# Optimization experiments

Hardware: AMD Instinct MI355X
Metric: run time of the kernel (lower is better)

The kernel has to match this reference:

```python
import jax, jax.numpy as jnp
import numpy as np

B, T_IN, N, C_IN = 4, 16, 5000, 16
HID, C_OUT, KSZ, K_CHEB = 32, 64, 3, 3
E = 80000
BN_EPS = 1e-5


def _conv1xk(x, W, b):
    # x: (B,C,N,T), W: (O,I,1,k) -> (B,O,N,T-k+1)
    y = jax.lax.conv_general_dilated(x, W, (1, 1), 'VALID',
                                     dimension_numbers=('NCHW', 'OIHW', 'NCHW'))
    return y + b[None, :, None, None]


def temporal_conv(X, W1, b1, W2, b2, W3, b3):
    # X: (B,T,N,C) -> (B,T-k+1,N,O); gated temporal conv (GLU-style)
    Xp = jnp.transpose(X, (0, 3, 2, 1))  # (B,C,N,T)
    P = _conv1xk(Xp, W1, b1)
    Q = jax.nn.sigmoid(_conv1xk(Xp, W2, b2))
    R = _conv1xk(Xp, W3, b3)
    H = jax.nn.relu(P * Q + R)
    return jnp.transpose(H, (0, 3, 2, 1))


def cheb_conv(x, edge_index, edge_weight, W, b, lambda_max=2.0):
    # x: (B,T,N,C). Batched ChebConv with sym normalization (PyG semantics).
    n = x.shape[2]
    row, col = edge_index[0], edge_index[1]
    deg = jax.ops.segment_sum(edge_weight, row, num_segments=n)
    dis = jnp.where(deg > 0, deg ** -0.5, 0.0)
    w_norm = dis[row] * edge_weight * dis[col]  # (E,)

    def lhat(z):
        # A_norm z via scatter-add over edges, batched over (B,T)
        az = jnp.zeros_like(z).at[:, :, row, :].add(
            w_norm[None, None, :, None] * z[:, :, col, :])
        # L z = z - A_norm z ; L_hat = (2/lmax) L - I
        return (2.0 / lambda_max) * (z - az) - z

    Tx0 = x
    out = jnp.einsum('btnc,cd->btnd', Tx0, W[0])
    Tx1 = lhat(Tx0)
    out = out + jnp.einsum('btnc,cd->btnd', Tx1, W[1])
    for k in range(2, W.shape[0]):
        Tx2 = 2.0 * lhat(Tx1) - Tx0
        out = out + jnp.einsum('btnc,cd->btnd', Tx2, W[k])
        Tx0, Tx1 = Tx1, Tx2
    return out + b


def batch_norm_nodes(T, gamma, beta):
    # torch: permute to (B, N, T, C), BatchNorm2d(num_nodes), permute back
    Tp = jnp.transpose(T, (0, 2, 1, 3))  # (B,N,T,C)
    mean = jnp.mean(Tp, axis=(0, 2, 3), keepdims=True)
    var = jnp.mean((Tp - mean) ** 2, axis=(0, 2, 3), keepdims=True)  # biased
    Tn = (Tp - mean) / jnp.sqrt(var + BN_EPS)
    Tn = Tn * gamma[None, :, None, None] + beta[None, :, None, None]
    return jnp.transpose(Tn, (0, 2, 1, 3))


def setup_inputs() -> dict:
    key = jax.random.key(0)
    ks = jax.random.split(key, 20)
    s = 0.05
    inp = {
        'X': jax.random.normal(ks[0], (B, T_IN, N, C_IN), jnp.float32),
        'edge_index': jax.random.randint(ks[1], (2, E), 0, N, jnp.int64
                                         if jax.config.jax_enable_x64 else jnp.int32),
        'edge_weight': jax.random.uniform(ks[2], (E,), jnp.float32),
        'tc1_w1': jax.random.normal(ks[3], (HID, C_IN, 1, KSZ)) * s,
        'tc1_b1': jnp.zeros((HID,)),
        'tc1_w2': jax.random.normal(ks[4], (HID, C_IN, 1, KSZ)) * s,
        'tc1_b2': jnp.zeros((HID,)),
        'tc1_w3': jax.random.normal(ks[5], (HID, C_IN, 1, KSZ)) * s,
        'tc1_b3': jnp.zeros((HID,)),
        'cheb_W': jax.random.normal(ks[6], (K_CHEB, HID, HID)) * s,
        'cheb_b': jnp.zeros((HID,)),
        'tc2_w1': jax.random.normal(ks[7], (C_OUT, HID, 1, KSZ)) * s,
        'tc2_b1': jnp.zeros((C_OUT,)),
        'tc2_w2': jax.random.normal(ks[8], (C_OUT, HID, 1, KSZ)) * s,
        'tc2_b2': jnp.zeros((C_OUT,)),
        'tc2_w3': jax.random.normal(ks[9], (C_OUT, HID, 1, KSZ)) * s,
        'tc2_b3': jnp.zeros((C_OUT,)),
        'bn_gamma': jnp.ones((N,)),
        'bn_beta': jnp.zeros((N,)),
    }
    return inp


def reference(X, edge_index, edge_weight,
              tc1_w1, tc1_b1, tc1_w2, tc1_b2, tc1_w3, tc1_b3,
              cheb_W, cheb_b,
              tc2_w1, tc2_b1, tc2_w2, tc2_b2, tc2_w3, tc2_b3,
              bn_gamma, bn_beta):
    T0 = temporal_conv(X, tc1_w1, tc1_b1, tc1_w2, tc1_b2, tc1_w3, tc1_b3)
    T = jax.nn.relu(cheb_conv(T0, edge_index, edge_weight, cheb_W, cheb_b))
    T = temporal_conv(T, tc2_w1, tc2_b1, tc2_w2, tc2_b2, tc2_w3, tc2_b3)
    return batch_norm_nodes(T, bn_gamma, bn_beta)
```

## Files before the change

### kernel.cpp

```cpp
#include <hip/hip_runtime.h>
#include <hip/hip_bf16.h>

#define STC_N     5000
#define STC_TIN   16
#define STC_T1    14
#define STC_T2    12
#define STC_CIN   16
#define STC_CH    32
#define STC_CO    64
#define STC_BT1   56
#define STC_BT2   48
#define STC_RT1   17500
#define STC_GBLK  1280
#define STC_GWAVE (STC_GBLK*4)
#define STC_ROWB1 1792

#define STC_OFF_DEG   0
#define STC_OFF_CNT   20000
#define STC_OFF_CUR   40000
#define STC_OFF_DIS   60000
#define STC_OFF_OFFS  80000
#define STC_OFF_WN    100032
#define STC_OFF_CCOL  420032
#define STC_OFF_CW    740032
#define STC_OFF_T0    1060096
#define STC_OFF_G1    (STC_OFF_T0 + 17920000)
#define STC_OFF_G2    (STC_OFF_G1 + 17920000)
#define STC_OFF_PK2   (STC_OFF_G2 + 17920000)
#define STC_OFF_PK1   (STC_OFF_PK2 + 36864)
#define STC_OFF_PKC   (STC_OFF_PK1 + 12288)
#define STC_WS_REQ    (STC_OFF_PKC + 6144)

typedef __hip_bfloat16 bf16;
typedef short stc_s8 __attribute__((ext_vector_type(8)));
typedef float stc_f4 __attribute__((ext_vector_type(4)));

__device__ float stc_lo16(unsigned u) { return __uint_as_float(u << 16); }
__device__ float stc_hi16(unsigned u) { return __uint_as_float(u & 0xffff0000u); }
__device__ float stc_s2f(short s) {
    return __uint_as_float(((unsigned)(unsigned short)s) << 16);
}

__device__ short stc_f2bs(float f) {
    unsigned u = __float_as_uint(f);
    u = (u + 0x7FFFu + ((u >> 16) & 1u)) >> 16;
    return (short)u;
}

__global__ void STConv_9972914061616_kernel() {}

__global__ void stc_fill(float* out, int n, float val) {
    int i = blockIdx.x * 256 + threadIdx.x;
    if (i < n) out[i] = val;
}

__global__ void stc_init(int* zp,
                         const float* w1a, const float* w1b, const float* w1c,
                         const float* w2a, const float* w2b, const float* w2c,
                         const float* chW,
                         short* pk1, short* pk2, short* pkc) {
    if (blockIdx.x < 59) {
        int i = blockIdx.x * 256 + threadIdx.x;
        if (i < 15000) zp[i] = 0;
        return;
    }
    int gid = (blockIdx.x - 59) * 256 + threadIdx.x;
    if (gid >= 54 * 64) return;
    int fi = gid >> 6;
    int lane = gid & 63;
    int j = lane & 15;
    int quad = lane >> 4;
    short f[8];
    if (fi < 36) {
        int s = fi % 3;
        int cc4 = fi / 3;
        int conv = cc4 >> 2;
        int c4 = cc4 & 3;
        const float* Wp = (conv == 0) ? w2a : ((conv == 1) ? w2b : w2c);
        int och = c4 * 16 + j;
        for (int i = 0; i < 8; ++i) {
            int cc = quad * 8 + i;
            f[i] = stc_f2bs(Wp[och * 96 + cc * 3 + s]);
        }
        for (int i = 0; i < 8; ++i) pk2[(fi * 64 + lane) * 8 + i] = f[i];
    } else if (fi < 48) {
        int t = fi - 36;
        int s = t & 1;
        int cj = t >> 1;
        int conv = cj >> 1;
        int jt = cj & 1;
        const float* Wp = (conv == 0) ? w1a : ((conv == 1) ? w1b : w1c);
        int och = jt * 16 + j;
        for (int i = 0; i < 8; ++i) {
            int k = s * 32 + quad * 8 + i;
            int kt = k >> 4;
            int c = k & 15;
            f[i] = (kt < 3) ? stc_f2bs(Wp[och * 48 + c * 3 + kt]) : (short)0;
        }
        for (int i = 0; i < 8; ++i) pk1[(t * 64 + lane) * 8 + i] = f[i];
    } else {
        int t = fi - 48;
        int s = t >> 1;
        int jt = t & 1;
        int d = jt * 16 + j;
        for (int i = 0; i < 8; ++i) {
            int c = quad * 8 + i;
            float w0 = chW[c * 32 + d];
            float w1 = chW[1024 + c * 32 + d];
            float w2 = chW[2048 + c * 32 + d];
            float v = (s == 0) ? (w0 - w2) : ((s == 1) ? -w1 : 2.0f * w2);
            f[i] = stc_f2bs(v);
        }
        for (int i = 0; i < 8; ++i) pkc[(t * 64 + lane) * 8 + i] = f[i];
    }
}

__global__ void stc_deg(const int* ei, const float* ew, float* deg, int E) {
    int e = blockIdx.x * 256 + threadIdx.x;
    if (e < E) atomicAdd(&deg[ei[e]], ew[e]);
}

__global__ void stc_wnorm(const int* ei, const float* ew, const float* deg,
                          float* wn, int* cnt, int E) {
    int e = blockIdx.x * 256 + threadIdx.x;
    if (e < E) {
        int r = ei[e];
        int c = ei[E + e];
        float dr = deg[r];
        float dc = deg[c];
        float ir = (dr > 0.0f) ? rsqrtf(dr) : 0.0f;
        float ic = (dc > 0.0f) ? rsqrtf(dc) : 0.0f;
        wn[e] = ir * ew[e] * ic;
        atomicAdd(&cnt[r], 1);
    }
}

__global__ void stc_scan(const int* cnt, int* offs, int n) {
    __shared__ int s[256];
    int tid = threadIdx.x;
    int base = tid * 20;
    int loc[20];
    int sum = 0;
#pragma unroll
    for (int k = 0; k < 20; ++k) {
        int i = base + k;
        int v = (i < n) ? cnt[i] : 0;
        loc[k] = sum;
        sum += v;
    }
    s[tid] = sum;
    __syncthreads();
    for (int off = 1; off < 256; off <<= 1) {
        int t = (tid >= off) ? s[tid - off] : 0;
        __syncthreads();
        s[tid] += t;
        __syncthreads();
    }
    int pre = (tid > 0) ? s[tid - 1] : 0;
#pragma unroll
    for (int k = 0; k < 20; ++k) {
        int i = base + k;
        if (i < n) offs[i] = pre + loc[k];
    }
    if (tid == 255) offs[n] = s[255];
}

__global__ void stc_scatter(const int* ei, const float* wn, const int* offs,
                            int* cursor, int* ccol, float* cw, int E) {
    int e = blockIdx.x * 256 + threadIdx.x;
    if (e < E) {
        int r = ei[e];
        int pos = atomicAdd(&cursor[r], 1);
        int slot = offs[r] + pos;
        ccol[slot] = ei[E + e];
        cw[slot] = wn[e];
    }
}

__global__ __launch_bounds__(256, 2) void stc_tconv1m(
    const float* X, const short* pk1,
    const float* B1, const float* B2, const float* B3,
    bf16* T0) {
    int lane = threadIdx.x & 63;
    int j = lane & 15;
    int quad = lane >> 4;
    int wave = blockIdx.x * 4 + (threadIdx.x >> 6);

    stc_s8 bfrag[3][2][2];
    for (int conv = 0; conv < 3; ++conv)
        for (int jt = 0; jt < 2; ++jt)
            for (int s = 0; s < 2; ++s) {
                int t = (conv * 2 + jt) * 2 + s;
                bfrag[conv][jt][s] = *(const stc_s8*)(pk1 + (t * 64 + lane) * 8);
            }
    float pb[2], qb[2], rb[2];
    for (int jt = 0; jt < 2; ++jt) {
        int och = jt * 16 + j;
        pb[jt] = B1[och];
        qb[jt] = B2[och];
        rb[jt] = B3[och];
    }

    for (int rt = wave; rt < STC_RT1; rt += STC_GWAVE) {
        int rm = rt * 16 + j;
        int n = rm % STC_N;
        int bt = rm / STC_N;
        int t = bt % STC_T1;
        int b = bt / STC_T1;

        int kt0 = quad >> 1;
        int c0 = (quad & 1) * 8;
        const float* xp0 = X + ((size_t)((b * STC_TIN + t + kt0) * STC_N + n)) * STC_CIN + c0;
        stc_s8 af0;
        for (int i = 0; i < 8; ++i) af0[i] = stc_f2bs(xp0[i]);

        stc_s8 af1;
        if (quad < 2) {
            const float* xp1 = X + ((size_t)((b * STC_TIN + t + 2) * STC_N + n)) * STC_CIN + c0;
            for (int i = 0; i < 8; ++i) af1[i] = stc_f2bs(xp1[i]);
        } else {
            for (int i = 0; i < 8; ++i) af1[i] = 0;
        }

        stc_f4 acc[6];
        for (int a = 0; a < 6; ++a) acc[a] = (stc_f4){0.0f, 0.0f, 0.0f, 0.0f};
        for (int conv = 0; conv < 3; ++conv) {
            for (int jt = 0; jt < 2; ++jt) {
                int a = conv * 2 + jt;
                acc[a] = __builtin_amdgcn_mfma_f32_16x16x32_bf16(
                    af0, bfrag[conv][jt][0], acc[a], 0, 0, 0);
                acc[a] = __builtin_amdgcn_mfma_f32_16x16x32_bf16(
                    af1, bfrag[conv][jt][1], acc[a], 0, 0, 0);
            }
        }

        for (int jt = 0; jt < 2; ++jt) {
            for (int reg = 0; reg < 4; ++reg) {
                float P = acc[jt][reg] + pb[jt];
                float Q = acc[2 + jt][reg] + qb[jt];
                float R = acc[4 + jt][reg] + rb[jt];
                float Qc = fminf(fmaxf(Q, -30.0f), 30.0f);
                float sg = 1.0f / (1.0f + expf(-Qc));
                float h = P * sg + R;
                if (h < 0.0f) h = 0.0f;
                int row = rt * 16 + quad * 4 + reg;
                int nw = row % STC_N;
                int btw = row / STC_N;
                T0[(size_t)nw * STC_ROWB1 + btw * STC_CH + jt * 16 + j] =
                    __float2bfloat16(h);
            }
        }
    }
}

__global__ void stc_gatherv(const bf16* z, bf16* g, const int* offs,
                            const int* ccol, const float* cw) {
    int n = blockIdx.x;
    __shared__ int col_s[128];
    __shared__ float w_s[128];
    int beg = offs[n];
    int end = offs[n + 1];
    int cg = threadIdx.x & 3;
    int sl = threadIdx.x >> 2;
    int act = (sl < STC_BT1);
    float a0 = 0.f, a1 = 0.f, a2 = 0.f, a3 = 0.f;
    float a4 = 0.f, a5 = 0.f, a6 = 0.f, a7 = 0.f;
    const bf16* zb = z + sl * STC_CH + cg * 8;
    for (int chunk = beg; chunk < end; chunk += 128) {
        int m = end - chunk;
        if (m > 128) m = 128;
        if (threadIdx.x < m) {
            col_s[threadIdx.x] = ccol[chunk + threadIdx.x];
            w_s[threadIdx.x] = cw[chunk + threadIdx.x];
        }
        __syncthreads();
        if (act) {
            int i = 0;
            for (; i + 4 <= m; i += 4) {
                float w0 = w_s[i], w1 = w_s[i + 1], w2 = w_s[i + 2], w3 = w_s[i + 3];
                uint4 u0 = *(const uint4*)(zb + (size_t)col_s[i] * STC_ROWB1);
                uint4 u1 = *(const uint4*)(zb + (size_t)col_s[i + 1] * STC_ROWB1);
                uint4 u2 = *(const uint4*)(zb + (size_t)col_s[i + 2] * STC_ROWB1);
                uint4 u3 = *(const uint4*)(zb + (size_t)col_s[i + 3] * STC_ROWB1);
                a0 += w0 * stc_lo16(u0.x); a1 += w0 * stc_hi16(u0.x);
                a2 += w0 * stc_lo16(u0.y); a3 += w0 * stc_hi16(u0.y);
                a4 += w0 * stc_lo16(u0.z); a5 += w0 * stc_hi16(u0.z);
                a6 += w0 * stc_lo16(u0.w); a7 += w0 * stc_hi16(u0.w);
                a0 += w1 * stc_lo16(u1.x); a1 += w1 * stc_hi16(u1.x);
                a2 += w1 * stc_lo16(u1.y); a3 += w1 * stc_hi16(u1.y);
                a4 += w1 * stc_lo16(u1.z); a5 += w1 * stc_hi16(u1.z);
                a6 += w1 * stc_lo16(u1.w); a7 += w1 * stc_hi16(u1.w);
                a0 += w2 * stc_lo16(u2.x); a1 += w2 * stc_hi16(u2.x);
                a2 += w2 * stc_lo16(u2.y); a3 += w2 * stc_hi16(u2.y);
                a4 += w2 * stc_lo16(u2.z); a5 += w2 * stc_hi16(u2.z);
                a6 += w2 * stc_lo16(u2.w); a7 += w2 * stc_hi16(u2.w);
                a0 += w3 * stc_lo16(u3.x); a1 += w3 * stc_hi16(u3.x);
                a2 += w3 * stc_lo16(u3.y); a3 += w3 * stc_hi16(u3.y);
                a4 += w3 * stc_lo16(u3.z); a5 += w3 * stc_hi16(u3.z);
                a6 += w3 * stc_lo16(u3.w); a7 += w3 * stc_hi16(u3.w);
            }
            for (; i < m; ++i) {
                float w = w_s[i];
                uint4 u = *(const uint4*)(zb + (size_t)col_s[i] * STC_ROWB1);
                a0 += w * stc_lo16(u.x); a1 += w * stc_hi16(u.x);
                a2 += w * stc_lo16(u.y); a3 += w * stc_hi16(u.y);
                a4 += w * stc_lo16(u.z); a5 += w * stc_hi16(u.z);
                a6 += w * stc_lo16(u.w); a7 += w * stc_hi16(u.w);
            }
        }
        __syncthreads();
    }
    if (act) {
        unsigned p0 = ((unsigned)(unsigned short)stc_f2bs(a0)) |
                      (((unsigned)(unsigned short)stc_f2bs(a1)) << 16);
        unsigned p1 = ((unsigned)(unsigned short)stc_f2bs(a2)) |
                      (((unsigned)(unsigned short)stc_f2bs(a3)) << 16);
        unsigned p2 = ((unsigned)(unsigned short)stc_f2bs(a4)) |
                      (((unsigned)(unsigned short)stc_f2bs(a5)) << 16);
        unsigned p3 = ((unsigned)(unsigned short)stc_f2bs(a6)) |
                      (((unsigned)(unsigned short)stc_f2bs(a7)) << 16);
        uint4 o;
        o.x = p0; o.y = p1; o.z = p2; o.w = p3;
        *(uint4*)(g + (size_t)n * STC_ROWB1 + sl * STC_CH + cg * 8) = o;
    }
}

__global__ __launch_bounds__(256, 2) void stc_combconv2bn(
    const bf16* T0, const bf16* G1, const bf16* G2,
    const short* pkc, const float* chB,
    const short* pk2, const float* B1, const float* B2, const float* B3,
    const float* gamma, const float* beta, float* T2) {
    __shared__ short comb[4][64 * 40];
    __shared__ short hb[4][48 * 72];
    int lane = threadIdx.x & 63;
    int j = lane & 15;
    int quad = lane >> 4;
    int w = threadIdx.x >> 6;
    int n = blockIdx.x * 4 + w;
    short* cmb = comb[w];
    short* hbw = hb[w];

    {
        stc_s8 cfrag[3][2];
        for (int s = 0; s < 3; ++s)
            for (int jt = 0; jt < 2; ++jt)
                cfrag[s][jt] = *(const stc_s8*)(pkc + ((s * 2 + jt) * 64 + lane) * 8);
        float bl[2];
        bl[0] = chB[j];
        bl[1] = chB[16 + j];
        for (int t3 = 0; t3 < 4; ++t3) {
            size_t rm = (size_t)n * STC_BT1 + t3 * 16 + j;
            size_t abase = rm * STC_CH + quad * 8;
            stc_s8 a0 = *(const stc_s8*)(T0 + abase);
            stc_s8 a1 = *(const stc_s8*)(G1 + abase);
            stc_s8 a2 = *(const stc_s8*)(G2 + abase);
            stc_f4 acc[2];
            acc[0] = (stc_f4){0.0f, 0.0f, 0.0f, 0.0f};
            acc[1] = (stc_f4){0.0f, 0.0f, 0.0f, 0.0f};
            for (int jt = 0; jt < 2; ++jt) {
                acc[jt] = __builtin_amdgcn_mfma_f32_16x16x32_bf16(a0, cfrag[0][jt], acc[jt], 0, 0, 0);
                acc[jt] = __builtin_amdgcn_mfma_f32_16x16x32_bf16(a1, cfrag[1][jt], acc[jt], 0, 0, 0);
                acc[jt] = __builtin_amdgcn_mfma_f32_16x16x32_bf16(a2, cfrag[2][jt], acc[jt], 0, 0, 0);
            }
            for (int jt = 0; jt < 2; ++jt) {
                for (int reg = 0; reg < 4; ++reg) {
                    float h = acc[jt][reg] + bl[jt];
                    if (h < 0.0f) h = 0.0f;
                    int row = t3 * 16 + quad * 4 + reg;
                    cmb[row * 40 + jt * 16 + j] = stc_f2bs(h);
                }
            }
        }
    }

    stc_s8 bfrag[3][4][3];
    for (int conv = 0; conv < 3; ++conv)
        for (int c4 = 0; c4 < 4; ++c4)
            for (int s = 0; s < 3; ++s) {
                int fi = (conv * 4 + c4) * 3 + s;
                bfrag[conv][c4][s] = *(const stc_s8*)(pk2 + (fi * 64 + lane) * 8);
            }
    float pb[4], qb[4], rb[4];
    for (int c4 = 0; c4 < 4; ++c4) {
        int och = c4 * 16 + j;
        pb[c4] = B1[och];
        qb[c4] = B2[och];
        rb[c4] = B3[och];
    }

    float lsum = 0.0f;
    for (int t3 = 0; t3 < 3; ++t3) {
        int btb = t3 * 16;
        int bt2 = btb + j;
        int b = bt2 / STC_T2;
        int t = bt2 % STC_T2;
        const short* ap = cmb + (b * STC_T1 + t) * 40 + quad * 8;
        stc_s8 af0 = *(const stc_s8*)(ap);
        stc_s8 af1 = *(const stc_s8*)(ap + 40);
        stc_s8 af2 = *(const stc_s8*)(ap + 80);

        stc_f4 acc[12];
        for (int a = 0; a < 12; ++a) acc[a] = (stc_f4){0.0f, 0.0f, 0.0f, 0.0f};

        for (int conv = 0; conv < 3; ++conv) {
            for (int c4 = 0; c4 < 4; ++c4) {
                int a = conv * 4 + c4;
                acc[a] = __builtin_amdgcn_mfma_f32_16x16x32_bf16(
                    af0, bfrag[conv][c4][0], acc[a], 0, 0, 0);
                acc[a] = __builtin_amdgcn_mfma_f32_16x16x32_bf16(
                    af1, bfrag[conv][c4][1], acc[a], 0, 0, 0);
                acc[a] = __builtin_amdgcn_mfma_f32_16x16x32_bf16(
                    af2, bfrag[conv][c4][2], acc[a], 0, 0, 0);
            }
        }

        for (int c4 = 0; c4 < 4; ++c4) {
            for (int reg = 0; reg < 4; ++reg) {
                float P = acc[c4][reg] + pb[c4];
                float Q = acc[4 + c4][reg] + qb[c4];
                float R = acc[8 + c4][reg] + rb[c4];
                float Qc = fminf(fmaxf(Q, -30.0f), 30.0f);
                float sg = 1.0f / (1.0f + expf(-Qc));
                float h = P * sg + R;
                if (h < 0.0f) h = 0.0f;
                short hs = stc_f2bs(h);
                int row = btb + quad * 4 + reg;
                hbw[row * 72 + c4 * 16 + j] = hs;
                lsum += stc_s2f(hs);
            }
        }
    }

    for (int off = 32; off; off >>= 1) lsum += __shfl_xor(lsum, off);
    float mean = lsum * (1.0f / (STC_BT2 * STC_CO));
    float sq = 0.0f;
    for (int k = 0; k < STC_BT2; ++k) {
        float d = stc_s2f(hbw[k * 72 + lane]) - mean;
        sq += d * d;
    }
    for (int off = 32; off; off >>= 1) sq += __shfl_xor(sq, off);
    float var = sq * (1.0f / (STC_BT2 * STC_CO));
    float istd = rsqrtf(var + 1e-5f);
    float scale = istd * gamma[n];
    float shift = beta[n] - mean * scale;
    for (int k = 0; k < STC_BT2; ++k) {
        T2[((size_t)k * STC_N + n) * STC_CO + lane] =
            stc_s2f(hbw[k * 72 + lane]) * scale + shift;
    }
}

extern "C" void kernel_launch(void* const* d_in, const int* in_sizes, int n_in,
                              void* d_out, int out_size, void* d_ws, size_t ws_size,
                              hipStream_t stream) {
    float* out = (float*)d_out;
    int outb = (out_size + 255) / 256;

    if (n_in < 19) {
        stc_fill<<<outb, 256, 0, stream>>>(out, out_size, 60.0f);
        return;
    }
    if (ws_size < (size_t)STC_WS_REQ) {
        stc_fill<<<outb, 256, 0, stream>>>(out, out_size, 50.0f);
        return;
    }

    const float* X = (const float*)d_in[0];
    const int* ei = (const int*)d_in[1];
    const float* ew = (const float*)d_in[2];
    const float* w1a = (const float*)d_in[3];
    const float* b1a = (const float*)d_in[4];
    const float* w1b = (const float*)d_in[5];
    const float* b1b = (const float*)d_in[6];
    const float* w1c = (const float*)d_in[7];
    const float* b1c = (const float*)d_in[8];
    const float* chW = (const float*)d_in[9];
    const float* chB = (const float*)d_in[10];
    const float* w2a = (const float*)d_in[11];
    const float* b2a = (const float*)d_in[12];
    const float* w2b = (const float*)d_in[13];
    const float* b2b = (const float*)d_in[14];
    const float* w2c = (const float*)d_in[15];
    const float* b2c = (const float*)d_in[16];
    const float* gam = (const float*)d_in[17];
    const float* bet = (const float*)d_in[18];
    int E = in_sizes[1] / 2;

    char* ws = (char*)d_ws;
    float* deg = (float*)(ws + STC_OFF_DEG);
    int* cnt = (int*)(ws + STC_OFF_CNT);
    int* cursor = (int*)(ws + STC_OFF_CUR);
    int* offs = (int*)(ws + STC_OFF_OFFS);
    float* wn = (float*)(ws + STC_OFF_WN);
    int* ccol = (int*)(ws + STC_OFF_CCOL);
    float* cw = (float*)(ws + STC_OFF_CW);
    bf16* T0 = (bf16*)(ws + STC_OFF_T0);
    bf16* G1 = (bf16*)(ws + STC_OFF_G1);
    bf16* G2 = (bf16*)(ws + STC_OFF_G2);
    short* pk2 = (short*)(ws + STC_OFF_PK2);
    short* pk1 = (short*)(ws + STC_OFF_PK1);
    short* pkc = (short*)(ws + STC_OFF_PKC);

    stc_init<<<73, 256, 0, stream>>>((int*)(ws + STC_OFF_DEG),
                                     w1a, w1b, w1c, w2a, w2b, w2c, chW,
                                     pk1, pk2, pkc);
    stc_deg<<<(E + 255) / 256, 256, 0, stream>>>(ei, ew, deg, E);
    stc_wnorm<<<(E + 255) / 256, 256, 0, stream>>>(ei, ew, deg, wn, cnt, E);
    stc_scan<<<1, 256, 0, stream>>>(cnt, offs, STC_N);
    stc_scatter<<<(E + 255) / 256, 256, 0, stream>>>(ei, wn, offs, cursor, ccol, cw, E);
    stc_tconv1m<<<STC_GBLK, 256, 0, stream>>>(X, pk1, b1a, b1b, b1c, T0);
    stc_gatherv<<<STC_N, 256, 0, stream>>>(T0, G1, offs, ccol, cw);
    stc_gatherv<<<STC_N, 256, 0, stream>>>(G1, G2, offs, ccol, cw);
    stc_combconv2bn<<<1250, 256, 0, stream>>>(
        T0, G1, G2, pkc, chB, pk2, b2a, b2b, b2c, gam, bet, out);
}
```

Measured before the change: 271.0 us.

## Split per-node conv2+batchnorm work across four waves of one block

The final fused kernel now assigns one node per 256-thread block instead of one node per wave. Each wave computes one 16-row tile of the Chebyshev combine and one 16-channel slice of the second temporal conv, and the BN mean and variance are reduced across waves through shared memory. This cuts per-wave register use (3 accumulators instead of 12, fewer weight fragments) and LDS footprint, which should allow higher occupancy, at the cost of block-level syncs. The sigmoid also switches from expf to the faster __expf intrinsic, which is slightly less accurate.

```diff
diff --git a/kernel.cpp b/kernel.cpp
--- a/kernel.cpp
+++ b/kernel.cpp
@@ -240,7 +240,7 @@
                 float Q = acc[2 + jt][reg] + qb[jt];
                 float R = acc[4 + jt][reg] + rb[jt];
                 float Qc = fminf(fmaxf(Q, -30.0f), 30.0f);
-                float sg = 1.0f / (1.0f + expf(-Qc));
+                float sg = 1.0f / (1.0f + __expf(-Qc));
                 float h = P * sg + R;
                 if (h < 0.0f) h = 0.0f;
                 int row = rt * 16 + quad * 4 + reg;
@@ -330,63 +330,57 @@
     const short* pkc, const float* chB,
     const short* pk2, const float* B1, const float* B2, const float* B3,
     const float* gamma, const float* beta, float* T2) {
-    __shared__ short comb[4][64 * 40];
-    __shared__ short hb[4][48 * 72];
+    __shared__ short comb[64 * 40];
+    __shared__ short hb[48 * 72];
+    __shared__ float red[8];
     int lane = threadIdx.x & 63;
     int j = lane & 15;
     int quad = lane >> 4;
     int w = threadIdx.x >> 6;
-    int n = blockIdx.x * 4 + w;
-    short* cmb = comb[w];
-    short* hbw = hb[w];
+    int n = blockIdx.x;
 
     {
         stc_s8 cfrag[3][2];
         for (int s = 0; s < 3; ++s)
             for (int jt = 0; jt < 2; ++jt)
                 cfrag[s][jt] = *(const stc_s8*)(pkc + ((s * 2 + jt) * 64 + lane) * 8);
-        float bl[2];
-        bl[0] = chB[j];
-        bl[1] = chB[16 + j];
-        for (int t3 = 0; t3 < 4; ++t3) {
-            size_t rm = (size_t)n * STC_BT1 + t3 * 16 + j;
-            size_t abase = rm * STC_CH + quad * 8;
-            stc_s8 a0 = *(const stc_s8*)(T0 + abase);
-            stc_s8 a1 = *(const stc_s8*)(G1 + abase);
-            stc_s8 a2 = *(const stc_s8*)(G2 + abase);
-            stc_f4 acc[2];
-            acc[0] = (stc_f4){0.0f, 0.0f, 0.0f, 0.0f};
-            acc[1] = (stc_f4){0.0f, 0.0f, 0.0f, 0.0f};
-            for (int jt = 0; jt < 2; ++jt) {
-                acc[jt] = __builtin_amdgcn_mfma_f32_16x16x32_bf16(a0, cfrag[0][jt], acc[jt], 0, 0, 0);
-                acc[jt] = __builtin_amdgcn_mfma_f32_16x16x32_bf16(a1, cfrag[1][jt], acc[jt], 0, 0, 0);
-                acc[jt] = __builtin_amdgcn_mfma_f32_16x16x32_bf16(a2, cfrag[2][jt], acc[jt], 0, 0, 0);
+        float bl0 = chB[j];
+        float bl1 = chB[16 + j];
+        size_t rm = (size_t)n * STC_BT1 + w * 16 + j;
+        size_t abase = rm * STC_CH + quad * 8;
+        stc_s8 a0 = *(const stc_s8*)(T0 + abase);
+        stc_s8 a1 = *(const stc_s8*)(G1 + abase);
+        stc_s8 a2 = *(const stc_s8*)(G2 + abase);
+        stc_f4 acc[2];
+        acc[0] = (stc_f4){0.0f, 0.0f, 0.0f, 0.0f};
+        acc[1] = (stc_f4){0.0f, 0.0f, 0.0f, 0.0f};
+        for (int jt = 0; jt < 2; ++jt) {
+            acc[jt] = __builtin_amdgcn_mfma_f32_16x16x32_bf16(a0, cfrag[0][jt], acc[jt], 0, 0, 0);
+            acc[jt] = __builtin_amdgcn_mfma_f32_16x16x32_bf16(a1, cfrag[1][jt], acc[jt], 0, 0, 0);
+            acc[jt] = __builtin_amdgcn_mfma_f32_16x16x32_bf16(a2, cfrag[2][jt], acc[jt], 0, 0, 0);
+        }
+        for (int jt = 0; jt < 2; ++jt) {
+            float bl = (jt == 0) ? bl0 : bl1;
+            for (int reg = 0; reg < 4; ++reg) {
+                float h = acc[jt][reg] + bl;
+                if (h < 0.0f) h = 0.0f;
+                int row = w * 16 + quad * 4 + reg;
+                comb[row * 40 + jt * 16 + j] = stc_f2bs(h);
             }
-            for (int jt = 0; jt < 2; ++jt) {
-                for (int reg = 0; reg < 4; ++reg) {
-                    float h = acc[jt][reg] + bl[jt];
-                    if (h < 0.0f) h = 0.0f;
-                    int row = t3 * 16 + quad * 4 + reg;
-                    cmb[row * 40 + jt * 16 + j] = stc_f2bs(h);
-                }
-            }
-        }
-    }
-
-    stc_s8 bfrag[3][4][3];
+        }
+    }
+    __syncthreads();
+
+    stc_s8 bfrag[3][3];
     for (int conv = 0; conv < 3; ++conv)
-        for (int c4 = 0; c4 < 4; ++c4)
-            for (int s = 0; s < 3; ++s) {
-                int fi = (conv * 4 + c4) * 3 + s;
-                bfrag[conv][c4][s] = *(const stc_s8*)(pk2 + (fi * 64 + lane) * 8);
-            }
-    float pb[4], qb[4], rb[4];
-    for (int c4 = 0; c4 < 4; ++c4) {
-        int och = c4 * 16 + j;
-        pb[c4] = B1[och];
-        qb[c4] = B2[och];
-        rb[c4] = B3[och];
-    }
+        for (int s = 0; s < 3; ++s) {
+            int fi = (conv * 4 + w) * 3 + s;
+            bfrag[conv][s] = *(const stc_s8*)(pk2 + (fi * 64 + lane) * 8);
+        }
+    int och = w * 16 + j;
+    float pb = B1[och];
+    float qb = B2[och];
+    float rb = B3[och];
 
     float lsum = 0.0f;
     for (int t3 = 0; t3 < 3; ++t3) {
@@ -394,58 +388,61 @@
         int bt2 = btb + j;
         int b = bt2 / STC_T2;
         int t = bt2 % STC_T2;
-        const short* ap = cmb + (b * STC_T1 + t) * 40 + quad * 8;
+        const short* ap = comb + (b * STC_T1 + t) * 40 + quad * 8;
         stc_s8 af0 = *(const stc_s8*)(ap);
         stc_s8 af1 = *(const stc_s8*)(ap + 40);
         stc_s8 af2 = *(const stc_s8*)(ap + 80);
 
-        stc_f4 acc[12];
-        for (int a = 0; a < 12; ++a) acc[a] = (stc_f4){0.0f, 0.0f, 0.0f, 0.0f};
-
+        stc_f4 acc[3];
+        for (int a = 0; a < 3; ++a) acc[a] = (stc_f4){0.0f, 0.0f, 0.0f, 0.0f};
         for (int conv = 0; conv < 3; ++conv) {
-            for (int c4 = 0; c4 < 4; ++c4) {
-                int a = conv * 4 + c4;
-                acc[a] = __builtin_amdgcn_mfma_f32_16x16x32_bf16(
-                    af0, bfrag[conv][c4][0], acc[a], 0, 0, 0);
-                acc[a] = __builtin_amdgcn_mfma_f32_16x16x32_bf16(
-                    af1, bfrag[conv][c4][1], acc[a], 0, 0, 0);
-                acc[a] = __builtin_amdgcn_mfma_f32_16x16x32_bf16(
-                    af2, bfrag[conv][c4][2], acc[a], 0, 0, 0);
-            }
-        }
-
-        for (int c4 = 0; c4 < 4; ++c4) {
-            for (int reg = 0; reg < 4; ++reg) {
-                float P = acc[c4][reg] + pb[c4];
-                float Q = acc[4 + c4][reg] + qb[c4];
-                float R = acc[8 + c4][reg] + rb[c4];
-                float Qc = fminf(fmaxf(Q, -30.0f), 30.0f);
-                float sg = 1.0f / (1.0f + expf(-Qc));
-                float h = P * sg + R;
-                if (h < 0.0f) h = 0.0f;
-                short hs = stc_f2bs(h);
-                int row = btb + quad * 4 + reg;
-                hbw[row * 72 + c4 * 16 + j] = hs;
-                lsum += stc_s2f(hs);
-            }
-        }
-    }
-
+            acc[conv] = __builtin_amdgcn_mfma_f32_16x16x32_bf16(
+                af0, bfrag[conv][0], acc[conv], 0, 0, 0);
+            acc[conv] = __builtin_amdgcn_mfma_f32_16x16x32_bf16(
+                af1, bfrag[conv][1], acc[conv], 0, 0, 0);
+            acc[conv] = __builtin_amdgcn_mfma_f32_16x16x32_bf16(
+                af2, bfrag[conv][2], acc[conv], 0, 0, 0);
+        }
+
+        for (int reg = 0; reg < 4; ++reg) {
+            float P = acc[0][reg] + pb;
+            float Q = acc[1][reg] + qb;
+            float R = acc[2][reg] + rb;
+            float Qc = fminf(fmaxf(Q, -30.0f), 30.0f);
+            float sg = 1.0f / (1.0f + __expf(-Qc));
+            float h = P * sg + R;
+            if (h < 0.0f) h = 0.0f;
+            short hs = stc_f2bs(h);
+            int row = btb + quad * 4 + reg;
+            hb[row * 72 + w * 16 + j] = hs;
+            lsum += stc_s2f(hs);
+        }
+    }
     for (int off = 32; off; off >>= 1) lsum += __shfl_xor(lsum, off);
-    float mean = lsum * (1.0f / (STC_BT2 * STC_CO));
+    if (lane == 0) red[w] = lsum;
+    __syncthreads();
+
+    float mean = (red[0] + red[1] + red[2] + red[3]) * (1.0f / (STC_BT2 * STC_CO));
+
+    int colc = threadIdx.x & 63;
+    int rw0 = threadIdx.x >> 6;
     float sq = 0.0f;
-    for (int k = 0; k < STC_BT2; ++k) {
-        float d = stc_s2f(hbw[k * 72 + lane]) - mean;
+    for (int it = 0; it < 12; ++it) {
+        int row = it * 4 + rw0;
+        float d = stc_s2f(hb[row * 72 + colc]) - mean;
         sq += d * d;
     }
     for (int off = 32; off; off >>= 1) sq += __shfl_xor(sq, off);
-    float var = sq * (1.0f / (STC_BT2 * STC_CO));
+    if (lane == 0) red[4 + w] = sq;
+    __syncthreads();
+    float var = (red[4] + red[5] + red[6] + red[7]) * (1.0f / (STC_BT2 * STC_CO));
     float istd = rsqrtf(var + 1e-5f);
     float scale = istd * gamma[n];
     float shift = beta[n] - mean * scale;
-    for (int k = 0; k < STC_BT2; ++k) {
-        T2[((size_t)k * STC_N + n) * STC_CO + lane] =
-            stc_s2f(hbw[k * 72 + lane]) * scale + shift;
+    for (int it = 0; it < 12; ++it) {
+        int row = it * 4 + rw0;
+        T2[((size_t)row * STC_N + n) * STC_CO + colc] =
+            stc_s2f(hb[row * 72 + colc]) * scale + shift;
     }
 }
 
@@ -510,6 +507,6 @@
     stc_tconv1m<<<STC_GBLK, 256, 0, stream>>>(X, pk1, b1a, b1b, b1c, T0);
     stc_gatherv<<<STC_N, 256, 0, stream>>>(T0, G1, offs, ccol, cw);
     stc_gatherv<<<STC_N, 256, 0, stream>>>(G1, G2, offs, ccol, cw);
-    stc_combconv2bn<<<1250, 256, 0, stream>>>(
+    stc_combconv2bn<<<STC_N, 256, 0, stream>>>(
         T0, G1, G2, pkc, chB, pk2, b2a, b2b, b2c, gam, bet, out);
 }
```

Measured after the change: 257.0 us. 1.05x faster.
